# Optimization experiments

Hardware: AMD Instinct MI355X
Metric: run time of the kernel (lower is better)

## Reference

```python
import jax, jax.numpy as jnp
import numpy as np

B, T, C = 2, 2048, 1024
N_HEAD, N_KV_HEAD, N_GLOBAL_HEAD = 16, 8, 8
HEAD_DIM = C // N_HEAD  # 64
Q_PER_KV = N_HEAD // N_KV_HEAD  # 2
N_GLOBAL_KV = N_GLOBAL_HEAD // Q_PER_KV  # 4
VE_GATE_CH = 32


def setup_inputs() -> dict:
    key = jax.random.key(0)
    ks = jax.random.split(key, 8)
    x = jax.random.normal(ks[0], (B, T, C), jnp.float32)
    ve = jax.random.normal(ks[1], (B, T, N_KV_HEAD * HEAD_DIM), jnp.float32)
    # rotary cos/sin: [T, 1, head_dim//2]
    half = HEAD_DIM // 2
    inv_freq = 1.0 / (10000.0 ** (np.arange(half, dtype=np.float32) / half))
    ang = np.arange(T, dtype=np.float32)[:, None] * inv_freq[None, :]
    cos = jnp.asarray(np.cos(ang))[:, None, :]
    sin = jnp.asarray(np.sin(ang))[:, None, :]
    s = 0.02
    Wq = jax.random.normal(ks[2], (C, N_HEAD * HEAD_DIM), jnp.float32) * s
    Wk = jax.random.normal(ks[3], (C, N_KV_HEAD * HEAD_DIM), jnp.float32) * s
    Wv = jax.random.normal(ks[4], (C, N_KV_HEAD * HEAD_DIM), jnp.float32) * s
    Wproj = jax.random.normal(ks[5], (C, C), jnp.float32) * s
    Wgate = jax.random.normal(ks[6], (VE_GATE_CH, N_KV_HEAD), jnp.float32) * s
    return {"x": x, "ve": ve, "cos": cos, "sin": sin, "Wq": Wq, "Wk": Wk,
            "Wv": Wv, "Wproj": Wproj, "Wgate": Wgate, "window": 512}


def _rope(x, cos, sin):
    # x: [B,T,H,D]; cos/sin: [T,1,D/2]
    d = x.shape[-1] // 2
    x1, x2 = x[..., :d], x[..., d:]
    return jnp.concatenate([x1 * cos + x2 * sin, -x1 * sin + x2 * cos], axis=-1)


def _rmsnorm(x):
    eps = jnp.finfo(x.dtype).eps
    return x * jax.lax.rsqrt(jnp.mean(x * x, axis=-1, keepdims=True) + eps)


def _attn(q, k, v, mask):
    # q,k,v: [B,T,H,D]; mask: [T,T] bool (True = allowed)
    scale = 1.0 / jnp.sqrt(jnp.asarray(q.shape[-1], q.dtype))
    scores = jnp.einsum('bqhd,bkhd->bhqk', q, k) * scale
    scores = jnp.where(mask[None, None], scores, jnp.finfo(scores.dtype).min)
    p = jax.nn.softmax(scores, axis=-1)
    return jnp.einsum('bhqk,bkhd->bqhd', p, v)


def reference(x, ve, cos, sin, Wq, Wk, Wv, Wproj, Wgate, window):
    q = (x @ Wq).reshape(B, T, N_HEAD, HEAD_DIM)
    k = (x @ Wk).reshape(B, T, N_KV_HEAD, HEAD_DIM)
    v = (x @ Wv).reshape(B, T, N_KV_HEAD, HEAD_DIM)
    # value-embedding gate
    gate = 2.0 * jax.nn.sigmoid(x[..., :VE_GATE_CH] @ Wgate)  # [B,T,n_kv]
    v = v + gate[..., None] * ve.reshape(B, T, N_KV_HEAD, HEAD_DIM)
    q, k = _rope(q, cos, sin), _rope(k, cos, sin)
    q, k = _rmsnorm(q), _rmsnorm(k)
    # split global / local heads
    qg, ql = q[:, :, :N_GLOBAL_HEAD], q[:, :, N_GLOBAL_HEAD:]
    kg, kl = k[:, :, :N_GLOBAL_KV], k[:, :, N_GLOBAL_KV:]
    vg, vl = v[:, :, :N_GLOBAL_KV], v[:, :, N_GLOBAL_KV:]
    # GQA: expand kv heads
    kg, vg = jnp.repeat(kg, Q_PER_KV, axis=2), jnp.repeat(vg, Q_PER_KV, axis=2)
    kl, vl = jnp.repeat(kl, Q_PER_KV, axis=2), jnp.repeat(vl, Q_PER_KV, axis=2)
    i = jnp.arange(T)[:, None]
    j = jnp.arange(T)[None, :]
    causal = j <= i
    local_mask = causal & (j >= i - window)  # flash window_size=(window, 0)
    yg = _attn(qg, kg, vg, causal)
    yl = _attn(ql, kl, vl, local_mask)
    y = jnp.concatenate([yg, yl], axis=2).reshape(B, T, C)
    return y @ Wproj
```

## Files before the change

kernel.cpp:

```cpp
#include <hip/hip_runtime.h>
#include <hip/hip_bf16.h>

#define BB 2
#define TT 2048
#define CC 1024
#define NH 16
#define NKV 8
#define HD 64

typedef __attribute__((ext_vector_type(8))) short short8;
typedef __attribute__((ext_vector_type(4))) float float4v;
typedef __attribute__((ext_vector_type(4))) unsigned int uint4v;

__device__ __forceinline__ ushort f2bf(float f) {
    __hip_bfloat16 h = __float2bfloat16(f);
    union { __hip_bfloat16 h; ushort u; } v; v.h = h; return v.u;
}
__device__ __forceinline__ float bf2f(ushort u) {
    union { unsigned int i; float f; } v; v.i = ((unsigned int)u) << 16; return v.f;
}

__device__ __forceinline__ float fexp2(float x) {
#if __has_builtin(__builtin_amdgcn_exp2f)
    return __builtin_amdgcn_exp2f(x);
#else
    return __expf(x * 0.69314718056f);
#endif
}

__device__ __forceinline__ void gload16(const ushort* g, ushort* l) {
    __builtin_amdgcn_global_load_lds(
        (const __attribute__((address_space(1))) unsigned int*)g,
        (__attribute__((address_space(3))) unsigned int*)l, 16, 0, 0);
}

__device__ __forceinline__ void transpose_tile(
    const float* __restrict__ src, ushort* __restrict__ dst,
    int Kd, int Nd, int kt, int nt, float* tile )
{
    const int tid = threadIdx.x;
    {
        int r = tid >> 2, c = (tid & 3) * 16;
        #pragma unroll
        for (int i = 0; i < 4; i++) {
            float4 v = *(const float4*)&src[(size_t)(kt + r) * Nd + nt + c + i * 4];
            tile[r * 65 + c + i * 4 + 0] = v.x;
            tile[r * 65 + c + i * 4 + 1] = v.y;
            tile[r * 65 + c + i * 4 + 2] = v.z;
            tile[r * 65 + c + i * 4 + 3] = v.w;
        }
    }
    __syncthreads();
    {
        int n = tid >> 2, k = (tid & 3) * 16;
        #pragma unroll
        for (int i = 0; i < 2; i++) {
            ushort u[8];
            #pragma unroll
            for (int j = 0; j < 8; j++) u[j] = f2bf(tile[(k + i * 8 + j) * 65 + n]);
            *(uint4*)&dst[(size_t)(nt + n) * Kd + kt + k + i * 8] = *(uint4*)u;
        }
    }
}

__global__ __launch_bounds__(256) void prep_kernel(
    const float* __restrict__ x, ushort* __restrict__ xb,
    const float* __restrict__ Wq, const float* __restrict__ Wk,
    const float* __restrict__ Wv, const float* __restrict__ Wproj,
    const float* __restrict__ wgate,
    ushort* __restrict__ WqkvT, ushort* __restrict__ WpT,
    float* __restrict__ gateP)
{
    __shared__ float tile[64 * 65];
    const int bid = blockIdx.x;
    if (bid < 4096) {
        int i = (bid * 256 + threadIdx.x) * 4;
        float4 v = *(const float4*)&x[i];
        xb[i + 0] = f2bf(v.x);
        xb[i + 1] = f2bf(v.y);
        xb[i + 2] = f2bf(v.z);
        xb[i + 3] = f2bf(v.w);
        {
            int g = threadIdx.x >> 5, ii = threadIdx.x & 31;
            float p = x[(size_t)bid * CC + ii] * wgate[ii * 8 + g];
            #pragma unroll
            for (int off = 16; off; off >>= 1) p += __shfl_down(p, off, 32);
            if (ii == 0) gateP[bid * 8 + g] = 2.f / (1.f + __expf(-p));
        }
        return;
    }
    int t = bid - 4096;
    if (t < 256) {
        transpose_tile(Wq, WqkvT, 1024, 1024, (t >> 4) * 64, (t & 15) * 64, tile);
    } else if (t < 384) {
        t -= 256;
        transpose_tile(Wk, WqkvT + (size_t)1024 * 1024, 1024, 512, (t >> 3) * 64, (t & 7) * 64, tile);
    } else if (t < 512) {
        t -= 384;
        transpose_tile(Wv, WqkvT + (size_t)1536 * 1024, 1024, 512, (t >> 3) * 64, (t & 7) * 64, tile);
    } else {
        t -= 512;
        transpose_tile(Wproj, WpT, 1024, 1024, (t >> 4) * 64, (t & 15) * 64, tile);
    }
}

template<int BM, int OBF16>
__global__ __launch_bounds__(256) void gemm_bt_kernel(
    const ushort* __restrict__ A, const ushort* __restrict__ Bt,
    void* __restrict__ Cp, int M, int N, int K, int ldc)
{
    constexpr int RT = BM / 32;
    __shared__ ushort As[BM][32];
    __shared__ ushort Bs[128][32];

    const int m0 = blockIdx.x * BM;
    const int n0 = blockIdx.y * 128;
    const int tid = threadIdx.x;
    const int lane = tid & 63;
    const int w = tid >> 6;
    const int lr = lane & 15, lc = lane >> 4;
    const int wm = (w >> 1) * (BM / 2), wn = (w & 1) * 64;

    float4v acc[RT][4] = {};

    for (int k0 = 0; k0 < K; k0 += 32) {
        #pragma unroll
        for (int s = 0; s < BM / 64; s++) {
            int rb = w * (BM / 4) + s * 16;
            gload16(&A[(size_t)(m0 + rb + (lane >> 2)) * K + k0 + (lane & 3) * 8], &As[rb][0]);
        }
        #pragma unroll
        for (int s = 0; s < 2; s++) {
            int rb = w * 32 + s * 16;
            gload16(&Bt[(size_t)(n0 + rb + (lane >> 2)) * K + k0 + (lane & 3) * 8], &Bs[rb][0]);
        }
        __syncthreads();

        short8 af[RT], bf[4];
        #pragma unroll
        for (int t = 0; t < RT; t++)
            af[t] = *(const short8*)&As[wm + t * 16 + lr][lc * 8];
        #pragma unroll
        for (int t = 0; t < 4; t++)
            bf[t] = *(const short8*)&Bs[wn + t * 16 + lr][lc * 8];
        #pragma unroll
        for (int rt = 0; rt < RT; rt++)
            #pragma unroll
            for (int ct = 0; ct < 4; ct++)
                acc[rt][ct] = __builtin_amdgcn_mfma_f32_16x16x32_bf16(af[rt], bf[ct], acc[rt][ct], 0, 0, 0);
        __syncthreads();
    }

    #pragma unroll
    for (int rt = 0; rt < RT; rt++)
        #pragma unroll
        for (int ct = 0; ct < 4; ct++)
            #pragma unroll
            for (int r = 0; r < 4; r++) {
                int row = m0 + wm + rt * 16 + lc * 4 + r;
                int col = n0 + wn + ct * 16 + lr;
                if (OBF16) ((ushort*)Cp)[(size_t)row * ldc + col] = f2bf(acc[rt][ct][r]);
                else       ((float*)Cp)[(size_t)row * ldc + col] = acc[rt][ct][r];
            }
}

__global__ __launch_bounds__(256) void gemm_qkv_kernel(
    const ushort* __restrict__ A, const ushort* __restrict__ Bt,
    const float* __restrict__ cosb, const float* __restrict__ sinb,
    const float* __restrict__ gateP, const float* __restrict__ ve,
    ushort* __restrict__ Qb, ushort* __restrict__ Kb, ushort* __restrict__ Vn)
{
    constexpr int K = 1024;
    __shared__ ushort As[128][32];
    __shared__ ushort Bs[128][32];

    const int m0 = blockIdx.x * 128;
    const int n0 = blockIdx.y * 128;
    const int tid = threadIdx.x;
    const int lane = tid & 63;
    const int w = tid >> 6;
    const int lr = lane & 15, lc = lane >> 4;
    const int wm = (w >> 1) * 64, wn = (w & 1) * 64;

    float4v acc[4][4] = {};

    for (int k0 = 0; k0 < K; k0 += 32) {
        #pragma unroll
        for (int s = 0; s < 2; s++) {
            int rb = w * 32 + s * 16;
            gload16(&A[(size_t)(m0 + rb + (lane >> 2)) * K + k0 + (lane & 3) * 8], &As[rb][0]);
            gload16(&Bt[(size_t)(n0 + rb + (lane >> 2)) * K + k0 + (lane & 3) * 8], &Bs[rb][0]);
        }
        __syncthreads();

        short8 af[4], bf[4];
        #pragma unroll
        for (int t = 0; t < 4; t++)
            af[t] = *(const short8*)&As[wm + t * 16 + lr][lc * 8];
        #pragma unroll
        for (int t = 0; t < 4; t++)
            bf[t] = *(const short8*)&Bs[wn + t * 16 + lr][lc * 8];
        #pragma unroll
        for (int rt = 0; rt < 4; rt++)
            #pragma unroll
            for (int ct = 0; ct < 4; ct++)
                acc[rt][ct] = __builtin_amdgcn_mfma_f32_16x16x32_bf16(af[rt], bf[ct], acc[rt][ct], 0, 0, 0);
        __syncthreads();
    }

    const int cg = n0 + wn;
    const int hh2 = cg >> 6;

    if (hh2 < 24) {
        #pragma unroll
        for (int rt = 0; rt < 4; rt++) {
            #pragma unroll
            for (int r = 0; r < 4; r++) {
                int row = m0 + wm + rt * 16 + lc * 4 + r;
                int b = row >> 11, t = row & 2047;
                float v0 = acc[rt][0][r], v1 = acc[rt][1][r];
                float v2 = acc[rt][2][r], v3 = acc[rt][3][r];
                const float* cp = &cosb[t * 32];
                const float* sp = &sinb[t * 32];
                float c0 = cp[lr], s0 = sp[lr];
                float c1 = cp[16 + lr], s1 = sp[16 + lr];
                float r0 = v0 * c0 + v2 * s0;
                float r1 = v1 * c1 + v3 * s1;
                float r2 = v2 * c0 - v0 * s0;
                float r3 = v3 * c1 - v1 * s1;
                float ss = (r0 * r0 + r1 * r1) + (r2 * r2 + r3 * r3);
                ss += __shfl_xor(ss, 1);
                ss += __shfl_xor(ss, 2);
                ss += __shfl_xor(ss, 4);
                ss += __shfl_xor(ss, 8);
                float sc = rsqrtf(ss * (1.f / 64.f) + 1.1920929e-07f);
                ushort* op = (hh2 < 16)
                    ? &Qb[(((size_t)b * NH + hh2) * TT + t) * HD]
                    : &Kb[(((size_t)b * NKV + (hh2 - 16)) * TT + t) * HD];
                op[lr]      = f2bf(r0 * sc);
                op[16 + lr] = f2bf(r1 * sc);
                op[32 + lr] = f2bf(r2 * sc);
                op[48 + lr] = f2bf(r3 * sc);
            }
        }
    } else {
        const int kvh = hh2 - 24;
        #pragma unroll
        for (int rt = 0; rt < 4; rt++) {
            #pragma unroll
            for (int r = 0; r < 4; r++) {
                int row = m0 + wm + rt * 16 + lc * 4 + r;
                int b = row >> 11, t = row & 2047;
                float g = gateP[row * 8 + kvh];
                const float* vp = &ve[(size_t)row * 512 + kvh * 64];
                ushort* op = &Vn[(((size_t)b * NKV + kvh) * TT + t) * HD];
                op[lr]      = f2bf(acc[rt][0][r] + g * vp[lr]);
                op[16 + lr] = f2bf(acc[rt][1][r] + g * vp[16 + lr]);
                op[32 + lr] = f2bf(acc[rt][2][r] + g * vp[32 + lr]);
                op[48 + lr] = f2bf(acc[rt][3][r] + g * vp[48 + lr]);
            }
        }
    }
}

__global__ __launch_bounds__(256) void v_transpose_kernel(
    const ushort* __restrict__ Vn, ushort* __restrict__ Vt)
{
    __shared__ ushort tile[64][72];
    const int t0 = blockIdx.x * 64;
    const int bh = blockIdx.y;
    const ushort* src = &Vn[(size_t)bh * TT * HD + (size_t)t0 * HD];
    ushort* dst = &Vt[(size_t)bh * HD * TT + t0];
    const int tid = threadIdx.x;
    {
        int r = tid >> 2, c = (tid & 3) * 16;
        #pragma unroll
        for (int i = 0; i < 2; i++)
            *(uint4*)&tile[r][c + i * 8] = *(const uint4*)&src[(size_t)r * HD + c + i * 8];
    }
    __syncthreads();
    {
        int d = tid >> 2, c = (tid & 3) * 16;
        #pragma unroll
        for (int i = 0; i < 2; i++) {
            ushort u[8];
            #pragma unroll
            for (int j = 0; j < 8; j++) u[j] = tile[c + i * 8 + j][d];
            *(uint4*)&dst[(size_t)d * TT + c + i * 8] = *(uint4*)u;
        }
    }
}

__global__ __launch_bounds__(256) void attn_kernel(
    const ushort* __restrict__ Qb, const ushort* __restrict__ Kb,
    const ushort* __restrict__ Vt, ushort* __restrict__ Yb,
    const int* __restrict__ winp)
{
    const int bid = blockIdx.x;
    const int p = bid & 7;
    const int rank = bid >> 3;
    const int rtype = rank >> 7;
    const int rr = rank & 127;
    const int qw = 63 - (rr >> 1);
    const int h = (rtype ? 8 : 0) + (p >> 1) * 2 + (rr & 1);
    const int b = p & 1;

    const int q0 = qw * 32;
    const int kvh = h >> 1;
    const bool local = (h >= 8);
    int window = *winp;
    if (window < 0 || window > TT) window = TT;
    const int tid = threadIdx.x;
    const int w = tid >> 6;
    const int lane = tid & 63;
    const int lr = lane & 15, lc = lane >> 4;

    __shared__ float4v Ol[4][4][64];
    __shared__ float Ll[4][16];

    const ushort* qbase = &Qb[(((size_t)b * NH + h) * TT + q0) * HD];
    short8 qf[2][2];
    #pragma unroll
    for (int rt = 0; rt < 2; rt++)
        #pragma unroll
        for (int xh = 0; xh < 2; xh++)
            qf[rt][xh] = *(const short8*)&qbase[(size_t)(rt * 16 + lr) * HD + xh * 32 + lc * 8];

    float4v o[2][4] = {};
    float l_[2] = {0.f, 0.f};

    const ushort* Kbase = &Kb[((size_t)b * NKV + kvh) * TT * HD];
    const ushort* Vbase = &Vt[((size_t)b * NKV + kvh) * HD * TT];

    const int qlast = q0 + 31;
    int jstart = 0;
    if (local) { int js = q0 - window; if (js > 0) jstart = js & ~63; }
    const int j0first = jstart + w * 64;

    const float ESC = 0.1803368801f;

    short8 kf[4][2];
    if (j0first <= qlast) {
        #pragma unroll
        for (int jt = 0; jt < 4; jt++) {
            const ushort* kp = &Kbase[(size_t)(j0first + jt * 16 + lr) * HD + lc * 8];
            kf[jt][0] = *(const short8*)kp;
            kf[jt][1] = *(const short8*)(kp + 32);
        }
    }

    for (int j0 = j0first; j0 <= qlast; j0 += 256) {
        short8 vf[4][2];
        #pragma unroll
        for (int ct = 0; ct < 4; ct++) {
            const ushort* vp = &Vbase[(size_t)(ct * 16 + lr) * TT + j0 + lc * 8];
            vf[ct][0] = *(const short8*)vp;
            vf[ct][1] = *(const short8*)(vp + 32);
        }
        short8 kn[4][2];
        const bool more = (j0 + 256 <= qlast);
        if (more) {
            #pragma unroll
            for (int jt = 0; jt < 4; jt++) {
                const ushort* kp = &Kbase[(size_t)(j0 + 256 + jt * 16 + lr) * HD + lc * 8];
                kn[jt][0] = *(const short8*)kp;
                kn[jt][1] = *(const short8*)(kp + 32);
            }
        }

        float4v st[2][4];
        #pragma unroll
        for (int jt = 0; jt < 4; jt++)
            #pragma unroll
            for (int rt = 0; rt < 2; rt++) {
                float4v z = {};
                z = __builtin_amdgcn_mfma_f32_16x16x32_bf16(kf[jt][0], qf[rt][0], z, 0, 0, 0);
                z = __builtin_amdgcn_mfma_f32_16x16x32_bf16(kf[jt][1], qf[rt][1], z, 0, 0, 0);
                st[rt][jt] = z;
            }

        const bool need_c = (j0 + 63 > q0);
        const bool need_w = local && (j0 < qlast - window);

        #pragma unroll
        for (int rt = 0; rt < 2; rt++) {
            const int qrow = q0 + rt * 16 + lr;
            float p4[4][4];
            if (need_c || need_w) {
                #pragma unroll
                for (int jt = 0; jt < 4; jt++)
                    #pragma unroll
                    for (int r = 0; r < 4; r++) {
                        int key = j0 + jt * 16 + lc * 4 + r;
                        bool ok = (key <= qrow) && (!local || key >= qrow - window);
                        p4[jt][r] = ok ? fexp2(st[rt][jt][r] * ESC) : 0.f;
                    }
            } else {
                #pragma unroll
                for (int jt = 0; jt < 4; jt++)
                    #pragma unroll
                    for (int r = 0; r < 4; r++)
                        p4[jt][r] = fexp2(st[rt][jt][r] * ESC);
            }
            float s0 = (p4[0][0] + p4[0][1]) + (p4[0][2] + p4[0][3]);
            float s1 = (p4[1][0] + p4[1][1]) + (p4[1][2] + p4[1][3]);
            float s2 = (p4[2][0] + p4[2][1]) + (p4[2][2] + p4[2][3]);
            float s3 = (p4[3][0] + p4[3][1]) + (p4[3][2] + p4[3][3]);
            l_[rt] += (s0 + s1) + (s2 + s3);

            unsigned int a0, a1, b0, b1, c0, c1, d0, d1;
            asm("v_cvt_pk_bf16_f32 %0, %1, %2" : "=v"(a0) : "v"(p4[0][0]), "v"(p4[0][1]));
            asm("v_cvt_pk_bf16_f32 %0, %1, %2" : "=v"(a1) : "v"(p4[0][2]), "v"(p4[0][3]));
            asm("v_cvt_pk_bf16_f32 %0, %1, %2" : "=v"(b0) : "v"(p4[1][0]), "v"(p4[1][1]));
            asm("v_cvt_pk_bf16_f32 %0, %1, %2" : "=v"(b1) : "v"(p4[1][2]), "v"(p4[1][3]));
            asm("v_cvt_pk_bf16_f32 %0, %1, %2" : "=v"(c0) : "v"(p4[2][0]), "v"(p4[2][1]));
            asm("v_cvt_pk_bf16_f32 %0, %1, %2" : "=v"(c1) : "v"(p4[2][2]), "v"(p4[2][3]));
            asm("v_cvt_pk_bf16_f32 %0, %1, %2" : "=v"(d0) : "v"(p4[3][0]), "v"(p4[3][1]));
            asm("v_cvt_pk_bf16_f32 %0, %1, %2" : "=v"(d1) : "v"(p4[3][2]), "v"(p4[3][3]));

            asm("v_permlane32_swap_b32 %0, %1" : "+v"(a0), "+v"(b0));
            asm("v_permlane16_swap_b32 %0, %1" : "+v"(a0), "+v"(b0));
            asm("v_permlane32_swap_b32 %0, %1" : "+v"(a1), "+v"(b1));
            asm("v_permlane16_swap_b32 %0, %1" : "+v"(a1), "+v"(b1));
            asm("v_permlane32_swap_b32 %0, %1" : "+v"(c0), "+v"(d0));
            asm("v_permlane16_swap_b32 %0, %1" : "+v"(c0), "+v"(d0));
            asm("v_permlane32_swap_b32 %0, %1" : "+v"(c1), "+v"(d1));
            asm("v_permlane16_swap_b32 %0, %1" : "+v"(c1), "+v"(d1));

            uint4v u0 = {a0, a1, b0, b1};
            uint4v u1 = {c0, c1, d0, d1};
            short8 P0 = __builtin_bit_cast(short8, u0);
            short8 P1 = __builtin_bit_cast(short8, u1);

            #pragma unroll
            for (int ct = 0; ct < 4; ct++) {
                o[rt][ct] = __builtin_amdgcn_mfma_f32_16x16x32_bf16(vf[ct][0], P0, o[rt][ct], 0, 0, 0);
                o[rt][ct] = __builtin_amdgcn_mfma_f32_16x16x32_bf16(vf[ct][1], P1, o[rt][ct], 0, 0, 0);
            }
        }

        if (more) {
            #pragma unroll
            for (int jt = 0; jt < 4; jt++) {
                kf[jt][0] = kn[jt][0];
                kf[jt][1] = kn[jt][1];
            }
        }
    }

    #pragma unroll
    for (int rt = 0; rt < 2; rt++) {
        l_[rt] += __shfl_xor(l_[rt], 16);
        l_[rt] += __shfl_xor(l_[rt], 32);
    }

    #pragma unroll
    for (int rt = 0; rt < 2; rt++) {
        #pragma unroll
        for (int ct = 0; ct < 4; ct++) Ol[w][ct][lane] = o[rt][ct];
        if (lc == 0) Ll[w][lr] = l_[rt];
        __syncthreads();

        {
            const int ct = w;
            float ltot = (Ll[0][lr] + Ll[1][lr]) + (Ll[2][lr] + Ll[3][lr]);
            float inv = 1.f / fmaxf(ltot, 1e-20f);
            float4v a0 = Ol[0][ct][lane], a1 = Ol[1][ct][lane];
            float4v a2 = Ol[2][ct][lane], a3 = Ol[3][ct][lane];
            int qrow = q0 + rt * 16 + lr;
            ushort4 u;
            u.x = f2bf(((a0[0] + a1[0]) + (a2[0] + a3[0])) * inv);
            u.y = f2bf(((a0[1] + a1[1]) + (a2[1] + a3[1])) * inv);
            u.z = f2bf(((a0[2] + a1[2]) + (a2[2] + a3[2])) * inv);
            u.w = f2bf(((a0[3] + a1[3]) + (a2[3] + a3[3])) * inv);
            *(ushort4*)&Yb[((size_t)b * TT + qrow) * CC + h * 64 + ct * 16 + lc * 4] = u;
        }
        if (rt == 0) __syncthreads();
    }
}

extern "C" void kernel_launch(void* const* d_in, const int* in_sizes, int n_in,
                              void* d_out, int out_size, void* d_ws, size_t ws_size,
                              hipStream_t stream) {
    (void)in_sizes; (void)n_in; (void)out_size; (void)ws_size;
    const float* x     = (const float*)d_in[0];
    const float* ve    = (const float*)d_in[1];
    const float* cosb  = (const float*)d_in[2];
    const float* sinb  = (const float*)d_in[3];
    const float* Wq    = (const float*)d_in[4];
    const float* Wk    = (const float*)d_in[5];
    const float* Wv    = (const float*)d_in[6];
    const float* Wproj = (const float*)d_in[7];
    const float* Wgate = (const float*)d_in[8];
    const int*   winp  = (const int*)d_in[9];
    float* out = (float*)d_out;

    char* ws = (char*)d_ws;
    ushort* Yb    = (ushort*)ws;
    float*  gateP = (float*)(ws + 8388608);
    ushort* Vnb   = (ushort*)(ws + 12582912);
    ushort* xb    = (ushort*)(ws + 33554432);
    ushort* WqkvT = (ushort*)(ws + 41943040);
    ushort* WpT   = (ushort*)(ws + 46137344);
    ushort* Qb    = (ushort*)(ws + 48234496);
    ushort* Kb    = (ushort*)(ws + 56623104);
    ushort* Vtb   = (ushort*)(ws + 60817408);

    dim3 blk(256);
    prep_kernel<<<dim3(4864), blk, 0, stream>>>(x, xb, Wq, Wk, Wv, Wproj, Wgate, WqkvT, WpT, gateP);
    gemm_qkv_kernel<<<dim3(32, 16), blk, 0, stream>>>(xb, WqkvT, cosb, sinb, gateP, ve, Qb, Kb, Vnb);
    v_transpose_kernel<<<dim3(TT / 64, BB * NKV), blk, 0, stream>>>(Vnb, Vtb);
    attn_kernel<<<dim3(2048), blk, 0, stream>>>(Qb, Kb, Vtb, Yb, winp);
    gemm_bt_kernel<64, 0><<<dim3(64, 8), blk, 0, stream>>>(Yb, WpT, out, 4096, 1024, 1024, 1024);
}
```

Baseline: 203.4 us.

## Process both GQA query heads per attention block to share K/V loads

Each attention block now handles both query heads that share one KV head, so the K and V fragments loaded from global memory are reused for two heads. The grid is halved from 2048 to 1024 blocks. This cuts redundant K/V global traffic. In exchange it doubles accumulator and Q-fragment register use, which may lower occupancy, and leaves fewer blocks to balance the causal workload.

```diff
diff --git a/kernel.cpp b/kernel.cpp
--- a/kernel.cpp
+++ b/kernel.cpp
@@ -299,15 +299,15 @@
     const int bid = blockIdx.x;
     const int p = bid & 7;
     const int rank = bid >> 3;
-    const int rtype = rank >> 7;
-    const int rr = rank & 127;
-    const int qw = 63 - (rr >> 1);
-    const int h = (rtype ? 8 : 0) + (p >> 1) * 2 + (rr & 1);
+    const int rtype = rank >> 6;
+    const int rr = rank & 63;
+    const int qw = 63 - rr;
+    const int h0 = (rtype ? 8 : 0) + (p >> 1) * 2;
     const int b = p & 1;
 
     const int q0 = qw * 32;
-    const int kvh = h >> 1;
-    const bool local = (h >= 8);
+    const int kvh = h0 >> 1;
+    const bool local = (h0 >= 8);
     int window = *winp;
     if (window < 0 || window > TT) window = TT;
     const int tid = threadIdx.x;
@@ -318,16 +318,19 @@
     __shared__ float4v Ol[4][4][64];
     __shared__ float Ll[4][16];
 
-    const ushort* qbase = &Qb[(((size_t)b * NH + h) * TT + q0) * HD];
-    short8 qf[2][2];
+    short8 qf[2][2][2];
     #pragma unroll
-    for (int rt = 0; rt < 2; rt++)
-        #pragma unroll
-        for (int xh = 0; xh < 2; xh++)
-            qf[rt][xh] = *(const short8*)&qbase[(size_t)(rt * 16 + lr) * HD + xh * 32 + lc * 8];
-
-    float4v o[2][4] = {};
-    float l_[2] = {0.f, 0.f};
+    for (int hh = 0; hh < 2; hh++) {
+        const ushort* qbase = &Qb[(((size_t)b * NH + h0 + hh) * TT + q0) * HD];
+        #pragma unroll
+        for (int rt = 0; rt < 2; rt++)
+            #pragma unroll
+            for (int xh = 0; xh < 2; xh++)
+                qf[hh][rt][xh] = *(const short8*)&qbase[(size_t)(rt * 16 + lr) * HD + xh * 32 + lc * 8];
+    }
+
+    float4v o[2][2][4] = {};
+    float l_[2][2] = {};
 
     const ushort* Kbase = &Kb[((size_t)b * NKV + kvh) * TT * HD];
     const ushort* Vbase = &Vt[((size_t)b * NKV + kvh) * HD * TT];
@@ -368,74 +371,77 @@
             }
         }
 
-        float4v st[2][4];
-        #pragma unroll
-        for (int jt = 0; jt < 4; jt++)
-            #pragma unroll
-            for (int rt = 0; rt < 2; rt++) {
-                float4v z = {};
-                z = __builtin_amdgcn_mfma_f32_16x16x32_bf16(kf[jt][0], qf[rt][0], z, 0, 0, 0);
-                z = __builtin_amdgcn_mfma_f32_16x16x32_bf16(kf[jt][1], qf[rt][1], z, 0, 0, 0);
-                st[rt][jt] = z;
-            }
-
         const bool need_c = (j0 + 63 > q0);
         const bool need_w = local && (j0 < qlast - window);
 
         #pragma unroll
-        for (int rt = 0; rt < 2; rt++) {
-            const int qrow = q0 + rt * 16 + lr;
-            float p4[4][4];
-            if (need_c || need_w) {
+        for (int hh = 0; hh < 2; hh++) {
+            float4v st[2][4];
+            #pragma unroll
+            for (int jt = 0; jt < 4; jt++)
                 #pragma unroll
-                for (int jt = 0; jt < 4; jt++)
+                for (int rt = 0; rt < 2; rt++) {
+                    float4v z = {};
+                    z = __builtin_amdgcn_mfma_f32_16x16x32_bf16(kf[jt][0], qf[hh][rt][0], z, 0, 0, 0);
+                    z = __builtin_amdgcn_mfma_f32_16x16x32_bf16(kf[jt][1], qf[hh][rt][1], z, 0, 0, 0);
+                    st[rt][jt] = z;
+                }
+
+            #pragma unroll
+            for (int rt = 0; rt < 2; rt++) {
+                const int qrow = q0 + rt * 16 + lr;
+                float p4[4][4];
+                if (need_c || need_w) {
                     #pragma unroll
-                    for (int r = 0; r < 4; r++) {
-                        int key = j0 + jt * 16 + lc * 4 + r;
-                        bool ok = (key <= qrow) && (!local || key >= qrow - window);
-                        p4[jt][r] = ok ? fexp2(st[rt][jt][r] * ESC) : 0.f;
-                    }
-            } else {
+                    for (int jt = 0; jt < 4; jt++)
+                        #pragma unroll
+                        for (int r = 0; r < 4; r++) {
+                            int key = j0 + jt * 16 + lc * 4 + r;
+                            bool ok = (key <= qrow) && (!local || key >= qrow - window);
+                            p4[jt][r] = ok ? fexp2(st[rt][jt][r] * ESC) : 0.f;
+                        }
+                } else {
+                    #pragma unroll
+                    for (int jt = 0; jt < 4; jt++)
+                        #pragma unroll
+                        for (int r = 0; r < 4; r++)
+                            p4[jt][r] = fexp2(st[rt][jt][r] * ESC);
+                }
+                float s0 = (p4[0][0] + p4[0][1]) + (p4[0][2] + p4[0][3]);
+                float s1 = (p4[1][0] + p4[1][1]) + (p4[1][2] + p4[1][3]);
+                float s2 = (p4[2][0] + p4[2][1]) + (p4[2][2] + p4[2][3]);
+                float s3 = (p4[3][0] + p4[3][1]) + (p4[3][2] + p4[3][3]);
+                l_[hh][rt] += (s0 + s1) + (s2 + s3);
+
+                unsigned int a0, a1, b0, b1, c0, c1, d0, d1;
+                asm("v_cvt_pk_bf16_f32 %0, %1, %2" : "=v"(a0) : "v"(p4[0][0]), "v"(p4[0][1]));
+                asm("v_cvt_pk_bf16_f32 %0, %1, %2" : "=v"(a1) : "v"(p4[0][2]), "v"(p4[0][3]));
+                asm("v_cvt_pk_bf16_f32 %0, %1, %2" : "=v"(b0) : "v"(p4[1][0]), "v"(p4[1][1]));
+                asm("v_cvt_pk_bf16_f32 %0, %1, %2" : "=v"(b1) : "v"(p4[1][2]), "v"(p4[1][3]));
+                asm("v_cvt_pk_bf16_f32 %0, %1, %2" : "=v"(c0) : "v"(p4[2][0]), "v"(p4[2][1]));
+                asm("v_cvt_pk_bf16_f32 %0, %1, %2" : "=v"(c1) : "v"(p4[2][2]), "v"(p4[2][3]));
+                asm("v_cvt_pk_bf16_f32 %0, %1, %2" : "=v"(d0) : "v"(p4[3][0]), "v"(p4[3][1]));
+                asm("v_cvt_pk_bf16_f32 %0, %1, %2" : "=v"(d1) : "v"(p4[3][2]), "v"(p4[3][3]));
+
+                asm("v_permlane32_swap_b32 %0, %1" : "+v"(a0), "+v"(b0));
+                asm("v_permlane16_swap_b32 %0, %1" : "+v"(a0), "+v"(b0));
+                asm("v_permlane32_swap_b32 %0, %1" : "+v"(a1), "+v"(b1));
+                asm("v_permlane16_swap_b32 %0, %1" : "+v"(a1), "+v"(b1));
+                asm("v_permlane32_swap_b32 %0, %1" : "+v"(c0), "+v"(d0));
+                asm("v_permlane16_swap_b32 %0, %1" : "+v"(c0), "+v"(d0));
+                asm("v_permlane32_swap_b32 %0, %1" : "+v"(c1), "+v"(d1));
+                asm("v_permlane16_swap_b32 %0, %1" : "+v"(c1), "+v"(d1));
+
+                uint4v u0 = {a0, a1, b0, b1};
+                uint4v u1 = {c0, c1, d0, d1};
+                short8 P0 = __builtin_bit_cast(short8, u0);
+                short8 P1 = __builtin_bit_cast(short8, u1);
+
                 #pragma unroll
-                for (int jt = 0; jt < 4; jt++)
-                    #pragma unroll
-                    for (int r = 0; r < 4; r++)
-                        p4[jt][r] = fexp2(st[rt][jt][r] * ESC);
-            }
-            float s0 = (p4[0][0] + p4[0][1]) + (p4[0][2] + p4[0][3]);
-            float s1 = (p4[1][0] + p4[1][1]) + (p4[1][2] + p4[1][3]);
-            float s2 = (p4[2][0] + p4[2][1]) + (p4[2][2] + p4[2][3]);
-            float s3 = (p4[3][0] + p4[3][1]) + (p4[3][2] + p4[3][3]);
-            l_[rt] += (s0 + s1) + (s2 + s3);
-
-            unsigned int a0, a1, b0, b1, c0, c1, d0, d1;
-            asm("v_cvt_pk_bf16_f32 %0, %1, %2" : "=v"(a0) : "v"(p4[0][0]), "v"(p4[0][1]));
-            asm("v_cvt_pk_bf16_f32 %0, %1, %2" : "=v"(a1) : "v"(p4[0][2]), "v"(p4[0][3]));
-            asm("v_cvt_pk_bf16_f32 %0, %1, %2" : "=v"(b0) : "v"(p4[1][0]), "v"(p4[1][1]));
-            asm("v_cvt_pk_bf16_f32 %0, %1, %2" : "=v"(b1) : "v"(p4[1][2]), "v"(p4[1][3]));
-            asm("v_cvt_pk_bf16_f32 %0, %1, %2" : "=v"(c0) : "v"(p4[2][0]), "v"(p4[2][1]));
-            asm("v_cvt_pk_bf16_f32 %0, %1, %2" : "=v"(c1) : "v"(p4[2][2]), "v"(p4[2][3]));
-            asm("v_cvt_pk_bf16_f32 %0, %1, %2" : "=v"(d0) : "v"(p4[3][0]), "v"(p4[3][1]));
-            asm("v_cvt_pk_bf16_f32 %0, %1, %2" : "=v"(d1) : "v"(p4[3][2]), "v"(p4[3][3]));
-
-            asm("v_permlane32_swap_b32 %0, %1" : "+v"(a0), "+v"(b0));
-            asm("v_permlane16_swap_b32 %0, %1" : "+v"(a0), "+v"(b0));
-            asm("v_permlane32_swap_b32 %0, %1" : "+v"(a1), "+v"(b1));
-            asm("v_permlane16_swap_b32 %0, %1" : "+v"(a1), "+v"(b1));
-            asm("v_permlane32_swap_b32 %0, %1" : "+v"(c0), "+v"(d0));
-            asm("v_permlane16_swap_b32 %0, %1" : "+v"(c0), "+v"(d0));
-            asm("v_permlane32_swap_b32 %0, %1" : "+v"(c1), "+v"(d1));
-            asm("v_permlane16_swap_b32 %0, %1" : "+v"(c1), "+v"(d1));
-
-            uint4v u0 = {a0, a1, b0, b1};
-            uint4v u1 = {c0, c1, d0, d1};
-            short8 P0 = __builtin_bit_cast(short8, u0);
-            short8 P1 = __builtin_bit_cast(short8, u1);
-
-            #pragma unroll
-            for (int ct = 0; ct < 4; ct++) {
-                o[rt][ct] = __builtin_amdgcn_mfma_f32_16x16x32_bf16(vf[ct][0], P0, o[rt][ct], 0, 0, 0);
-                o[rt][ct] = __builtin_amdgcn_mfma_f32_16x16x32_bf16(vf[ct][1], P1, o[rt][ct], 0, 0, 0);
+                for (int ct = 0; ct < 4; ct++) {
+                    o[hh][rt][ct] = __builtin_amdgcn_mfma_f32_16x16x32_bf16(vf[ct][0], P0, o[hh][rt][ct], 0, 0, 0);
+                    o[hh][rt][ct] = __builtin_amdgcn_mfma_f32_16x16x32_bf16(vf[ct][1], P1, o[hh][rt][ct], 0, 0, 0);
+                }
             }
         }
 
@@ -449,33 +455,39 @@
     }
 
     #pragma unroll
-    for (int rt = 0; rt < 2; rt++) {
-        l_[rt] += __shfl_xor(l_[rt], 16);
-        l_[rt] += __shfl_xor(l_[rt], 32);
-    }
+    for (int hh = 0; hh < 2; hh++)
+        #pragma unroll
+        for (int rt = 0; rt < 2; rt++) {
+            l_[hh][rt] += __shfl_xor(l_[hh][rt], 16);
+            l_[hh][rt] += __shfl_xor(l_[hh][rt], 32);
+        }
 
     #pragma unroll
-    for (int rt = 0; rt < 2; rt++) {
-        #pragma unroll
-        for (int ct = 0; ct < 4; ct++) Ol[w][ct][lane] = o[rt][ct];
-        if (lc == 0) Ll[w][lr] = l_[rt];
-        __syncthreads();
-
-        {
-            const int ct = w;
-            float ltot = (Ll[0][lr] + Ll[1][lr]) + (Ll[2][lr] + Ll[3][lr]);
-            float inv = 1.f / fmaxf(ltot, 1e-20f);
-            float4v a0 = Ol[0][ct][lane], a1 = Ol[1][ct][lane];
-            float4v a2 = Ol[2][ct][lane], a3 = Ol[3][ct][lane];
-            int qrow = q0 + rt * 16 + lr;
-            ushort4 u;
-            u.x = f2bf(((a0[0] + a1[0]) + (a2[0] + a3[0])) * inv);
-            u.y = f2bf(((a0[1] + a1[1]) + (a2[1] + a3[1])) * inv);
-            u.z = f2bf(((a0[2] + a1[2]) + (a2[2] + a3[2])) * inv);
-            u.w = f2bf(((a0[3] + a1[3]) + (a2[3] + a3[3])) * inv);
-            *(ushort4*)&Yb[((size_t)b * TT + qrow) * CC + h * 64 + ct * 16 + lc * 4] = u;
-        }
-        if (rt == 0) __syncthreads();
+    for (int hh = 0; hh < 2; hh++) {
+        const int h = h0 + hh;
+        #pragma unroll
+        for (int rt = 0; rt < 2; rt++) {
+            #pragma unroll
+            for (int ct = 0; ct < 4; ct++) Ol[w][ct][lane] = o[hh][rt][ct];
+            if (lc == 0) Ll[w][lr] = l_[hh][rt];
+            __syncthreads();
+
+            {
+                const int ct = w;
+                float ltot = (Ll[0][lr] + Ll[1][lr]) + (Ll[2][lr] + Ll[3][lr]);
+                float inv = 1.f / fmaxf(ltot, 1e-20f);
+                float4v a0 = Ol[0][ct][lane], a1 = Ol[1][ct][lane];
+                float4v a2 = Ol[2][ct][lane], a3 = Ol[3][ct][lane];
+                int qrow = q0 + rt * 16 + lr;
+                ushort4 u;
+                u.x = f2bf(((a0[0] + a1[0]) + (a2[0] + a3[0])) * inv);
+                u.y = f2bf(((a0[1] + a1[1]) + (a2[1] + a3[1])) * inv);
+                u.z = f2bf(((a0[2] + a1[2]) + (a2[2] + a3[2])) * inv);
+                u.w = f2bf(((a0[3] + a1[3]) + (a2[3] + a3[3])) * inv);
+                *(ushort4*)&Yb[((size_t)b * TT + qrow) * CC + h * 64 + ct * 16 + lc * 4] = u;
+            }
+            if (!(hh == 1 && rt == 1)) __syncthreads();
+        }
     }
 }
 
@@ -510,6 +522,6 @@
     prep_kernel<<<dim3(4864), blk, 0, stream>>>(x, xb, Wq, Wk, Wv, Wproj, Wgate, WqkvT, WpT, gateP);
     gemm_qkv_kernel<<<dim3(32, 16), blk, 0, stream>>>(xb, WqkvT, cosb, sinb, gateP, ve, Qb, Kb, Vnb);
     v_transpose_kernel<<<dim3(TT / 64, BB * NKV), blk, 0, stream>>>(Vnb, Vtb);
-    attn_kernel<<<dim3(2048), blk, 0, stream>>>(Qb, Kb, Vtb, Yb, winp);
+    attn_kernel<<<dim3(1024), blk, 0, stream>>>(Qb, Kb, Vtb, Yb, winp);
     gemm_bt_kernel<64, 0><<<dim3(64, 8), blk, 0, stream>>>(Yb, WpT, out, 4096, 1024, 1024, 1024);
 }
```

Result: no change. 204.2 us (+0.4%).
